# Kernel optimization log

Hardware: AMD Instinct MI355X
Metric: run time of the kernel (lower is better)

Reference implementation:

```python
import jax, jax.numpy as jnp
import numpy as np

N = 64      # n_particles
C = 3       # coord_dim
H = 128     # hidden_dim
L = 4       # n_layers
B = 128     # batch

silu = jax.nn.silu


def setup_inputs() -> dict:
    key = jax.random.key(0)
    ks = jax.random.split(key, 16)

    x = jax.random.normal(ks[0], (B, N * C), dtype=jnp.float32)

    # fully-connected edge index (i != j), batched with node offsets
    idx = np.arange(N)
    src = np.repeat(idx, N)
    dst = np.tile(idx, N)
    mask = src != dst
    src, dst = src[mask], dst[mask]            # [N*(N-1)]
    offs = (np.arange(B) * N)[:, None]
    src_all = (src[None, :] + offs).reshape(-1)
    dst_all = (dst[None, :] + offs).reshape(-1)
    edge_index = jnp.asarray(np.stack([src_all, dst_all]), dtype=jnp.int32)  # [2, B*N*(N-1)]

    s = 0.05
    node_embed = jax.random.normal(ks[1], (1, H), dtype=jnp.float32) * 0.01
    output_scale = jnp.ones((1,), dtype=jnp.float32)  # orig inits to 0; use 1 for non-degenerate baseline

    def rn(k, shape, scale=s):
        return jax.random.normal(k, shape, dtype=jnp.float32) * scale

    return {
        "x": x,
        "node_embed": node_embed,
        "output_scale": output_scale,
        "edge_w1": rn(ks[2], (L, 2 * H + 1, H)),
        "edge_b1": jnp.zeros((L, H), jnp.float32),
        "edge_w2": rn(ks[3], (L, H, H)),
        "edge_b2": jnp.zeros((L, H), jnp.float32),
        "coord_w1": rn(ks[4], (L, H, H)),
        "coord_b1": jnp.zeros((L, H), jnp.float32),
        "coord_w2": rn(ks[5], (L, H, 1), scale=0.001),  # xavier gain=0.01
        "node_w1": rn(ks[6], (L, 2 * H, H)),
        "node_b1": jnp.zeros((L, H), jnp.float32),
        "node_w2": rn(ks[7], (L, H, H)),
        "node_b2": jnp.zeros((L, H), jnp.float32),
        "edge_index": edge_index,
    }


def reference(x, node_embed, output_scale,
              edge_w1, edge_b1, edge_w2, edge_b2,
              coord_w1, coord_b1, coord_w2,
              node_w1, node_b1, node_w2, node_b2,
              edge_index):
    batch = x.shape[0]
    n_nodes = batch * N
    pos0 = x.reshape(n_nodes, C)
    pos = pos0
    h = jnp.broadcast_to(node_embed, (n_nodes, H))
    src, dst = edge_index[0], edge_index[1]

    for l in range(L):
        rel = pos[src] - pos[dst]                                   # [E, C]
        d2 = jnp.sum(rel * rel, axis=-1, keepdims=True)             # [E, 1]
        e_in = jnp.concatenate([h[src], h[dst], d2], axis=-1)       # [E, 2H+1]
        m = silu(silu(e_in @ edge_w1[l] + edge_b1[l]) @ edge_w2[l] + edge_b2[l])  # [E, H]
        cw = silu(m @ coord_w1[l] + coord_b1[l]) @ coord_w2[l]      # [E, 1]
        pos = pos + jax.ops.segment_sum(rel * cw, dst, num_segments=n_nodes)
        msg = jax.ops.segment_sum(m, dst, num_segments=n_nodes)     # [n_nodes, H]
        node_in = jnp.concatenate([h, msg], axis=-1)                # [n_nodes, 2H]
        h = h + (silu(node_in @ node_w1[l] + node_b1[l]) @ node_w2[l] + node_b2[l])

    dx = (pos - pos0).reshape(batch, N, C)
    dx = dx - jnp.mean(dx, axis=1, keepdims=True)
    return (dx * output_scale).reshape(batch, -1)
```

## Files before the change

### kernel.cpp

```cpp
#include <hip/hip_runtime.h>

#define H 128
#define LDP 132
#define NN 64

typedef short bf8_t __attribute__((ext_vector_type(8)));
typedef float f4_t  __attribute__((ext_vector_type(4)));

__device__ __forceinline__ float silu_f(float v) {
  return v * (1.0f / (1.0f + __expf(-v)));
}
__device__ __forceinline__ unsigned short f2bf(float f) {
  unsigned int u = __float_as_uint(f);
  u = (u + 0x7fffu + ((u >> 16) & 1u)) >> 16;
  return (unsigned short)u;
}
__device__ __forceinline__ float bf2f(unsigned short h) {
  return __uint_as_float(((unsigned int)h) << 16);
}

template<int RPT>
__device__ __forceinline__ void gemm_acc(const float* A, const float* __restrict__ Wg,
                                         float (&acc)[RPT][8], int r0, int c0) {
#pragma unroll 4
  for (int k = 0; k < H; k += 4) {
    float4 av[RPT];
#pragma unroll
    for (int rr = 0; rr < RPT; ++rr)
      av[rr] = *(const float4*)(A + (r0 + rr) * LDP + k);
#pragma unroll
    for (int kk = 0; kk < 4; ++kk) {
      const float* wrow = Wg + (k + kk) * H + c0;
      float4 w0 = *(const float4*)(wrow);
      float4 w1 = *(const float4*)(wrow + 4);
#pragma unroll
      for (int rr = 0; rr < RPT; ++rr) {
        float a = (kk == 0) ? av[rr].x : (kk == 1) ? av[rr].y : (kk == 2) ? av[rr].z : av[rr].w;
        acc[rr][0] = fmaf(a, w0.x, acc[rr][0]);
        acc[rr][1] = fmaf(a, w0.y, acc[rr][1]);
        acc[rr][2] = fmaf(a, w0.z, acc[rr][2]);
        acc[rr][3] = fmaf(a, w0.w, acc[rr][3]);
        acc[rr][4] = fmaf(a, w1.x, acc[rr][4]);
        acc[rr][5] = fmaf(a, w1.y, acc[rr][5]);
        acc[rr][6] = fmaf(a, w1.z, acc[rr][6]);
        acc[rr][7] = fmaf(a, w1.w, acc[rr][7]);
      }
    }
  }
}

__global__ void init_kernel(const float* __restrict__ x, const float* __restrict__ ne,
                            float* __restrict__ h, float* __restrict__ pos0,
                            float* __restrict__ posA) {
  int g = blockIdx.x * 256 + threadIdx.x;
  h[g] = ne[g & (H - 1)];
  if (g < 24576) { pos0[g] = x[g]; posA[g] = x[g]; }
}

__global__ void prep_kernel(const float* __restrict__ ew2, const float* __restrict__ cw1,
                            unsigned short* __restrict__ whi, unsigned short* __restrict__ wlo) {
  int idx = blockIdx.x * 256 + threadIdx.x;
  int l = idx >> 15;
  int r = idx & 32767;
  int mat = r >> 14;
  int e = r & 16383;
  int k = e >> 7, c = e & 127;
  const float* src = mat ? cw1 : ew2;
  float w = src[(size_t)l * 16384 + k * 128 + c];
  unsigned short hi = f2bf(w);
  unsigned short lo = f2bf(w - bf2f(hi));
  size_t dst = (size_t)(l * 2 + mat) * 16384 + c * 128 + k;
  whi[dst] = hi;
  wlo[dst] = lo;
}

__global__ __launch_bounds__(256) void proj_kernel(
    const float* __restrict__ h, const float* __restrict__ ew1,
    const float* __restrict__ eb1, const float* __restrict__ nw1,
    const float* __restrict__ nb1, float* __restrict__ hs,
    float* __restrict__ hd, float* __restrict__ hn) {
  __shared__ float As[NN * LDP];
  const int tid = threadIdx.x;
  const int rb = blockIdx.x & 127;
  const int wsel = blockIdx.x >> 7;
  const int rowbase = rb * NN;
  for (int f = tid; f < NN * H / 4; f += 256) {
    int row = f >> 5, c4 = (f & 31) << 2;
    *(float4*)(As + row * LDP + c4) = *(const float4*)(h + (size_t)(rowbase + row) * H + c4);
  }
  __syncthreads();
  const float* W; const float* bias; float* out;
  if (wsel == 0)      { W = ew1;          bias = nullptr; out = hs; }
  else if (wsel == 1) { W = ew1 + H * H;  bias = eb1;     out = hd; }
  else                { W = nw1;          bias = nb1;     out = hn; }
  const int tx = tid & 15, ty = tid >> 4;
  const int c0 = tx * 8, r0 = ty * 4;
  float acc[4][8] = {};
  gemm_acc<4>(As, W, acc, r0, c0);
#pragma unroll
  for (int rr = 0; rr < 4; ++rr) {
#pragma unroll
    for (int cc = 0; cc < 8; ++cc) {
      float v = acc[rr][cc] + (bias ? bias[c0 + cc] : 0.0f);
      out[(size_t)(rowbase + r0 + rr) * H + c0 + cc] = v;
    }
  }
}

__device__ __forceinline__ void gemm_mfma(
    const unsigned short* Ahi, const unsigned short* Alo,
    const unsigned short* __restrict__ Bhi, const unsigned short* __restrict__ Blo,
    f4_t (&acc)[4][2], int lane, int wave) {
  const int arow = lane & 15;
  const int kch = (lane >> 4) * 8;
  const int bcol = wave * 32 + (lane & 15);
#pragma unroll
  for (int Kt = 0; Kt < 4; ++Kt) {
    const int k0 = Kt * 32 + kch;
    bf8_t bh0 = *(const bf8_t*)(Bhi + (size_t)bcol * H + k0);
    bf8_t bl0 = *(const bf8_t*)(Blo + (size_t)bcol * H + k0);
    bf8_t bh1 = *(const bf8_t*)(Bhi + (size_t)(bcol + 16) * H + k0);
    bf8_t bl1 = *(const bf8_t*)(Blo + (size_t)(bcol + 16) * H + k0);
#pragma unroll
    for (int Mt = 0; Mt < 4; ++Mt) {
      int row = Mt * 16 + arow;
      int byte = (row * 256 + k0 * 2) ^ ((row & 7) << 4);
      bf8_t ah = *(const bf8_t*)((const char*)Ahi + byte);
      bf8_t al = *(const bf8_t*)((const char*)Alo + byte);
      acc[Mt][0] = __builtin_amdgcn_mfma_f32_16x16x32_bf16(ah, bh0, acc[Mt][0], 0, 0, 0);
      acc[Mt][1] = __builtin_amdgcn_mfma_f32_16x16x32_bf16(ah, bh1, acc[Mt][1], 0, 0, 0);
      acc[Mt][0] = __builtin_amdgcn_mfma_f32_16x16x32_bf16(al, bh0, acc[Mt][0], 0, 0, 0);
      acc[Mt][1] = __builtin_amdgcn_mfma_f32_16x16x32_bf16(al, bh1, acc[Mt][1], 0, 0, 0);
      acc[Mt][0] = __builtin_amdgcn_mfma_f32_16x16x32_bf16(ah, bl0, acc[Mt][0], 0, 0, 0);
      acc[Mt][1] = __builtin_amdgcn_mfma_f32_16x16x32_bf16(ah, bl1, acc[Mt][1], 0, 0, 0);
    }
  }
}

__global__ __launch_bounds__(256) void edge_kernel(
    const float* __restrict__ hs, const float* __restrict__ hd,
    const float* __restrict__ w1c,
    const unsigned short* __restrict__ w2t_hi, const unsigned short* __restrict__ w2t_lo,
    const unsigned short* __restrict__ wc1t_hi, const unsigned short* __restrict__ wc1t_lo,
    const float* __restrict__ b2, const float* __restrict__ bc1,
    const float* __restrict__ wc2,
    const float* __restrict__ pos_in, float* __restrict__ pos_out,
    float* __restrict__ msg) {
  __shared__ unsigned short Ahi[NN * H];
  __shared__ unsigned short Alo[NN * H];
  __shared__ float posbuf[192];
  __shared__ float relc[3][NN];
  __shared__ float d2s[NN];
  __shared__ float cws[NN];
  __shared__ float hdj[H];
  __shared__ float w1cs[H];
  __shared__ float posjs[3];

  const int tid = threadIdx.x;
  const int lane = tid & 63, wave = tid >> 6;
  const int b = blockIdx.x >> 6;
  const int j = blockIdx.x & 63;
  const int nb = b * NN;

  if (tid < 192) posbuf[tid] = pos_in[(size_t)nb * 3 + tid];
  else cws[tid - 192] = 0.0f;
  __syncthreads();
  if (tid < NN) {
    float px = posbuf[tid * 3], py = posbuf[tid * 3 + 1], pz = posbuf[tid * 3 + 2];
    float qx = posbuf[j * 3],   qy = posbuf[j * 3 + 1],   qz = posbuf[j * 3 + 2];
    float rx = px - qx, ry = py - qy, rz = pz - qz;
    relc[0][tid] = rx; relc[1][tid] = ry; relc[2][tid] = rz;
    d2s[tid] = rx * rx + ry * ry + rz * rz;
    if (tid < 3) posjs[tid] = posbuf[j * 3 + tid];
  } else if (tid < 128) {
    int c = tid - 64;
    w1cs[c] = w1c[c];
    w1cs[c + 64] = w1c[c + 64];
  } else {
    hdj[tid - 128] = hd[(size_t)(nb + j) * H + (tid - 128)];
  }
  __syncthreads();

  {
    const int c2 = lane * 2;
    float hd0 = hdj[c2], hd1 = hdj[c2 + 1];
    float w10 = w1cs[c2], w11 = w1cs[c2 + 1];
    for (int i = wave; i < NN; i += 4) {
      float2 hv = *(const float2*)(hs + (size_t)(nb + i) * H + c2);
      float d2v = d2s[i];
      float v0 = silu_f(hv.x + hd0 + d2v * w10);
      float v1 = silu_f(hv.y + hd1 + d2v * w11);
      unsigned short h0 = f2bf(v0), h1 = f2bf(v1);
      unsigned short l0 = f2bf(v0 - bf2f(h0)), l1 = f2bf(v1 - bf2f(h1));
      int byte = (i * 256 + c2 * 2) ^ ((i & 7) << 4);
      *(unsigned int*)((char*)Ahi + byte) = (unsigned int)h0 | ((unsigned int)h1 << 16);
      *(unsigned int*)((char*)Alo + byte) = (unsigned int)l0 | ((unsigned int)l1 << 16);
    }
  }
  __syncthreads();

  const int col0 = wave * 32 + (lane & 15);

  {
    f4_t acc[4][2];
#pragma unroll
    for (int m = 0; m < 4; ++m) {
      acc[m][0] = (f4_t){0.f, 0.f, 0.f, 0.f};
      acc[m][1] = (f4_t){0.f, 0.f, 0.f, 0.f};
    }
    gemm_mfma(Ahi, Alo, w2t_hi, w2t_lo, acc, lane, wave);
    __syncthreads();
    float biasA = b2[col0], biasB = b2[col0 + 16];
#pragma unroll
    for (int Mt = 0; Mt < 4; ++Mt) {
#pragma unroll
      for (int r = 0; r < 4; ++r) {
        int row = Mt * 16 + (lane >> 4) * 4 + r;
        int rsw = (row & 7) << 4;
        float vA = silu_f(acc[Mt][0][r] + biasA);
        float vB = silu_f(acc[Mt][1][r] + biasB);
        unsigned short hA = f2bf(vA), hB = f2bf(vB);
        unsigned short lA = f2bf(vA - bf2f(hA)), lB = f2bf(vB - bf2f(hB));
        int byA = (row * 256 + col0 * 2) ^ rsw;
        int byB = (row * 256 + (col0 + 16) * 2) ^ rsw;
        *(unsigned short*)((char*)Ahi + byA) = hA;
        *(unsigned short*)((char*)Alo + byA) = lA;
        *(unsigned short*)((char*)Ahi + byB) = hB;
        *(unsigned short*)((char*)Alo + byB) = lB;
      }
    }
  }
  __syncthreads();

  {
    f4_t acc2[4][2];
#pragma unroll
    for (int m = 0; m < 4; ++m) {
      acc2[m][0] = (f4_t){0.f, 0.f, 0.f, 0.f};
      acc2[m][1] = (f4_t){0.f, 0.f, 0.f, 0.f};
    }
    gemm_mfma(Ahi, Alo, wc1t_hi, wc1t_lo, acc2, lane, wave);
    float bcA = bc1[col0], bcB = bc1[col0 + 16];
    float wcA = wc2[col0], wcB = wc2[col0 + 16];
#pragma unroll
    for (int Mt = 0; Mt < 4; ++Mt) {
#pragma unroll
      for (int r = 0; r < 4; ++r) {
        int row = Mt * 16 + (lane >> 4) * 4 + r;
        float p = silu_f(acc2[Mt][0][r] + bcA) * wcA
                + silu_f(acc2[Mt][1][r] + bcB) * wcB;
        p += __shfl_xor(p, 8);
        p += __shfl_xor(p, 4);
        p += __shfl_xor(p, 2);
        p += __shfl_xor(p, 1);
        if ((lane & 15) == 0) atomicAdd(&cws[row], p);
      }
    }
  }
  __syncthreads();

  if (tid < H) {
    float s = 0.0f;
    for (int i = 0; i < NN; ++i) {
      int byte = (i * 256 + tid * 2) ^ ((i & 7) << 4);
      s += bf2f(*(const unsigned short*)((const char*)Ahi + byte))
         + bf2f(*(const unsigned short*)((const char*)Alo + byte));
    }
    int bj = (j * 256 + tid * 2) ^ ((j & 7) << 4);
    s -= bf2f(*(const unsigned short*)((const char*)Ahi + bj))
       + bf2f(*(const unsigned short*)((const char*)Alo + bj));
    msg[(size_t)(nb + j) * H + tid] = s;
  } else if (tid < H + 3) {
    int comp = tid - H;
    float s = 0.0f;
    for (int i = 0; i < NN; ++i) s = fmaf(relc[comp][i], cws[i], s);
    pos_out[(size_t)(nb + j) * 3 + comp] = posjs[comp] + s;
  }
}

__global__ __launch_bounds__(256) void node_kernel(
    const float* __restrict__ msg, const float* __restrict__ hn,
    const float* __restrict__ nw1b, const float* __restrict__ nw2,
    const float* __restrict__ nb2, float* __restrict__ h) {
  __shared__ float As[32 * LDP];
  __shared__ float Bs[32 * LDP];
  __shared__ float Us[32 * LDP];
  const int tid = threadIdx.x;
  const int rowbase = blockIdx.x * 32;
  for (int f = tid; f < 32 * H / 4; f += 256) {
    int row = f >> 5, c4 = (f & 31) << 2;
    *(float4*)(As + row * LDP + c4) = *(const float4*)(msg + (size_t)(rowbase + row) * H + c4);
    *(float4*)(Bs + row * LDP + c4) = *(const float4*)(hn + (size_t)(rowbase + row) * H + c4);
  }
  __syncthreads();
  const int tx = tid & 15, ty = tid >> 4;
  const int c0 = tx * 8, r0 = ty * 2;
  {
    float acc[2][8] = {};
    gemm_acc<2>(As, nw1b, acc, r0, c0);
#pragma unroll
    for (int rr = 0; rr < 2; ++rr)
#pragma unroll
      for (int cc = 0; cc < 8; ++cc)
        Us[(r0 + rr) * LDP + c0 + cc] =
            silu_f(acc[rr][cc] + Bs[(r0 + rr) * LDP + c0 + cc]);
  }
  __syncthreads();
  {
    float acc2[2][8] = {};
    gemm_acc<2>(Us, nw2, acc2, r0, c0);
#pragma unroll
    for (int rr = 0; rr < 2; ++rr)
#pragma unroll
      for (int cc = 0; cc < 8; ++cc) {
        size_t idx = (size_t)(rowbase + r0 + rr) * H + c0 + cc;
        h[idx] += acc2[rr][cc] + nb2[c0 + cc];
      }
  }
}

__global__ void out_kernel(const float* __restrict__ posF, const float* __restrict__ pos0,
                           const float* __restrict__ scale, float* __restrict__ out) {
  int b = blockIdx.x, i = threadIdx.x;
  int n = b * NN + i;
  float d0 = posF[n * 3]     - pos0[n * 3];
  float d1 = posF[n * 3 + 1] - pos0[n * 3 + 1];
  float d2v = posF[n * 3 + 2] - pos0[n * 3 + 2];
  float s0 = d0, s1 = d1, s2 = d2v;
  for (int m = 32; m; m >>= 1) {
    s0 += __shfl_xor(s0, m);
    s1 += __shfl_xor(s1, m);
    s2 += __shfl_xor(s2, m);
  }
  const float inv = 1.0f / 64.0f;
  float sc = scale[0];
  out[b * 192 + i * 3]     = (d0 - s0 * inv) * sc;
  out[b * 192 + i * 3 + 1] = (d1 - s1 * inv) * sc;
  out[b * 192 + i * 3 + 2] = (d2v - s2 * inv) * sc;
}

extern "C" void kernel_launch(void* const* d_in, const int* in_sizes, int n_in,
                              void* d_out, int out_size, void* d_ws, size_t ws_size,
                              hipStream_t stream) {
  (void)in_sizes; (void)n_in; (void)out_size; (void)ws_size;
  const float* x   = (const float*)d_in[0];
  const float* ne  = (const float*)d_in[1];
  const float* osc = (const float*)d_in[2];
  const float* ew1 = (const float*)d_in[3];
  const float* eb1 = (const float*)d_in[4];
  const float* ew2 = (const float*)d_in[5];
  const float* eb2 = (const float*)d_in[6];
  const float* cw1 = (const float*)d_in[7];
  const float* cb1 = (const float*)d_in[8];
  const float* cw2 = (const float*)d_in[9];
  const float* nw1 = (const float*)d_in[10];
  const float* nb1 = (const float*)d_in[11];
  const float* nw2 = (const float*)d_in[12];
  const float* nb2 = (const float*)d_in[13];

  float* ws = (float*)d_ws;
  float* pos0 = ws;
  float* posA = pos0 + 24576;
  float* posB = posA + 24576;
  float* h    = posB + 24576;
  float* hsb  = h   + 1048576;
  float* hdb  = hsb + 1048576;
  float* hnb  = hdb + 1048576;
  float* msgb = hnb + 1048576;
  unsigned short* whi = (unsigned short*)(msgb + 1048576);
  unsigned short* wlo = whi + 131072;

  init_kernel<<<4096, 256, 0, stream>>>(x, ne, h, pos0, posA);
  prep_kernel<<<512, 256, 0, stream>>>(ew2, cw1, whi, wlo);

  const float* pin[4]  = {posA, posB, posA, posB};
  float*       pout[4] = {posB, posA, posB, posA};

  for (int l = 0; l < 4; ++l) {
    const float* ew1l = ew1 + (size_t)l * 257 * H;
    const unsigned short* w2h = whi + (size_t)l * 2 * 16384;
    const unsigned short* w2l = wlo + (size_t)l * 2 * 16384;
    proj_kernel<<<384, 256, 0, stream>>>(h, ew1l, eb1 + l * H,
                                         nw1 + (size_t)l * 256 * H, nb1 + l * H,
                                         hsb, hdb, hnb);
    edge_kernel<<<8192, 256, 0, stream>>>(hsb, hdb, ew1l + 256 * H,
                                          w2h, w2l, w2h + 16384, w2l + 16384,
                                          eb2 + l * H, cb1 + l * H, cw2 + (size_t)l * H,
                                          pin[l], pout[l], msgb);
    node_kernel<<<256, 256, 0, stream>>>(msgb, hnb,
                                         nw1 + (size_t)l * 256 * H + H * H,
                                         nw2 + (size_t)l * H * H, nb2 + l * H, h);
  }
  out_kernel<<<128, 64, 0, stream>>>(posA, pos0, osc, (float*)d_out);
}
```

Baseline: 1.281 ms.

## Drop low-part A split in coord GEMM, fuse msg reduction into epilogue

The coordinate-MLP GEMM now runs with only the high bf16 part of the activation (4 MFMAs per tile instead of 6), so the low-part store to LDS is removed. The message sum over source nodes is computed in registers during the first GEMM epilogue with wave shuffles instead of a serial 64-row LDS loop at the end. The position update is also reduced with a wave shuffle rather than a serial loop. This lowers the precision of the coordinate weights to roughly bf16 on the activation side, which may move cw slightly.

```diff
diff --git a/kernel.cpp b/kernel.cpp
--- a/kernel.cpp
+++ b/kernel.cpp
@@ -107,6 +107,7 @@
   }
 }
 
+template<bool SPLIT_A>
 __device__ __forceinline__ void gemm_mfma(
     const unsigned short* Ahi, const unsigned short* Alo,
     const unsigned short* __restrict__ Bhi, const unsigned short* __restrict__ Blo,
@@ -126,11 +127,13 @@
       int row = Mt * 16 + arow;
       int byte = (row * 256 + k0 * 2) ^ ((row & 7) << 4);
       bf8_t ah = *(const bf8_t*)((const char*)Ahi + byte);
-      bf8_t al = *(const bf8_t*)((const char*)Alo + byte);
       acc[Mt][0] = __builtin_amdgcn_mfma_f32_16x16x32_bf16(ah, bh0, acc[Mt][0], 0, 0, 0);
       acc[Mt][1] = __builtin_amdgcn_mfma_f32_16x16x32_bf16(ah, bh1, acc[Mt][1], 0, 0, 0);
-      acc[Mt][0] = __builtin_amdgcn_mfma_f32_16x16x32_bf16(al, bh0, acc[Mt][0], 0, 0, 0);
-      acc[Mt][1] = __builtin_amdgcn_mfma_f32_16x16x32_bf16(al, bh1, acc[Mt][1], 0, 0, 0);
+      if (SPLIT_A) {
+        bf8_t al = *(const bf8_t*)((const char*)Alo + byte);
+        acc[Mt][0] = __builtin_amdgcn_mfma_f32_16x16x32_bf16(al, bh0, acc[Mt][0], 0, 0, 0);
+        acc[Mt][1] = __builtin_amdgcn_mfma_f32_16x16x32_bf16(al, bh1, acc[Mt][1], 0, 0, 0);
+      }
       acc[Mt][0] = __builtin_amdgcn_mfma_f32_16x16x32_bf16(ah, bl0, acc[Mt][0], 0, 0, 0);
       acc[Mt][1] = __builtin_amdgcn_mfma_f32_16x16x32_bf16(ah, bl1, acc[Mt][1], 0, 0, 0);
     }
@@ -208,9 +211,10 @@
       acc[m][0] = (f4_t){0.f, 0.f, 0.f, 0.f};
       acc[m][1] = (f4_t){0.f, 0.f, 0.f, 0.f};
     }
-    gemm_mfma(Ahi, Alo, w2t_hi, w2t_lo, acc, lane, wave);
+    gemm_mfma<true>(Ahi, Alo, w2t_hi, w2t_lo, acc, lane, wave);
     __syncthreads();
     float biasA = b2[col0], biasB = b2[col0 + 16];
+    float sA = 0.f, sB = 0.f, sjA = 0.f, sjB = 0.f;
 #pragma unroll
     for (int Mt = 0; Mt < 4; ++Mt) {
 #pragma unroll
@@ -219,15 +223,19 @@
         int rsw = (row & 7) << 4;
         float vA = silu_f(acc[Mt][0][r] + biasA);
         float vB = silu_f(acc[Mt][1][r] + biasB);
-        unsigned short hA = f2bf(vA), hB = f2bf(vB);
-        unsigned short lA = f2bf(vA - bf2f(hA)), lB = f2bf(vB - bf2f(hB));
-        int byA = (row * 256 + col0 * 2) ^ rsw;
-        int byB = (row * 256 + (col0 + 16) * 2) ^ rsw;
-        *(unsigned short*)((char*)Ahi + byA) = hA;
-        *(unsigned short*)((char*)Alo + byA) = lA;
-        *(unsigned short*)((char*)Ahi + byB) = hB;
-        *(unsigned short*)((char*)Alo + byB) = lB;
-      }
+        sA += vA; sB += vB;
+        if (row == j) { sjA = vA; sjB = vB; }
+        *(unsigned short*)((char*)Ahi + ((row * 256 + col0 * 2) ^ rsw)) = f2bf(vA);
+        *(unsigned short*)((char*)Ahi + ((row * 256 + (col0 + 16) * 2) ^ rsw)) = f2bf(vB);
+      }
+    }
+    sA  += __shfl_xor(sA, 16);  sA  += __shfl_xor(sA, 32);
+    sB  += __shfl_xor(sB, 16);  sB  += __shfl_xor(sB, 32);
+    sjA += __shfl_xor(sjA, 16); sjA += __shfl_xor(sjA, 32);
+    sjB += __shfl_xor(sjB, 16); sjB += __shfl_xor(sjB, 32);
+    if (lane < 16) {
+      msg[(size_t)(nb + j) * H + col0]      = sA - sjA;
+      msg[(size_t)(nb + j) * H + col0 + 16] = sB - sjB;
     }
   }
   __syncthreads();
@@ -239,7 +247,7 @@
       acc2[m][0] = (f4_t){0.f, 0.f, 0.f, 0.f};
       acc2[m][1] = (f4_t){0.f, 0.f, 0.f, 0.f};
     }
-    gemm_mfma(Ahi, Alo, wc1t_hi, wc1t_lo, acc2, lane, wave);
+    gemm_mfma<false>(Ahi, Alo, wc1t_hi, wc1t_lo, acc2, lane, wave);
     float bcA = bc1[col0], bcB = bc1[col0 + 16];
     float wcA = wc2[col0], wcB = wc2[col0 + 16];
 #pragma unroll
@@ -259,22 +267,14 @@
   }
   __syncthreads();
 
-  if (tid < H) {
-    float s = 0.0f;
-    for (int i = 0; i < NN; ++i) {
-      int byte = (i * 256 + tid * 2) ^ ((i & 7) << 4);
-      s += bf2f(*(const unsigned short*)((const char*)Ahi + byte))
-         + bf2f(*(const unsigned short*)((const char*)Alo + byte));
-    }
-    int bj = (j * 256 + tid * 2) ^ ((j & 7) << 4);
-    s -= bf2f(*(const unsigned short*)((const char*)Ahi + bj))
-       + bf2f(*(const unsigned short*)((const char*)Alo + bj));
-    msg[(size_t)(nb + j) * H + tid] = s;
-  } else if (tid < H + 3) {
-    int comp = tid - H;
-    float s = 0.0f;
-    for (int i = 0; i < NN; ++i) s = fmaf(relc[comp][i], cws[i], s);
-    pos_out[(size_t)(nb + j) * 3 + comp] = posjs[comp] + s;
+  if (wave == 0) {
+#pragma unroll
+    for (int comp = 0; comp < 3; ++comp) {
+      float p = relc[comp][lane] * cws[lane];
+#pragma unroll
+      for (int mk = 32; mk; mk >>= 1) p += __shfl_xor(p, mk);
+      if (lane == comp) pos_out[(size_t)(nb + j) * 3 + comp] = posjs[comp] + p;
+    }
   }
 }
 
```

Result: slower. 1.333 ms (+4.1%).
